# Performance work log

Measured on AMD Instinct MI355X. Metric: run time of the kernel, lower is better.

The kernel has to match this reference:

```python
import jax
import jax.numpy as jnp
from jax import lax
import numpy as np

B, C, Hsp, Wsp = 16, 256, 64, 64
E, HID = 4, 128          # num_experts, expert_hidden
RH = 128                 # router_hidden
TOP_K = 1
EPS = 1e-9


def setup_inputs() -> dict:
    key = jax.random.key(0)
    ks = jax.random.split(key, 8)
    s = lambda *shape: 1.0 / np.sqrt(shape[-1])
    x = jax.random.normal(ks[0], (B, C, Hsp, Wsp), dtype=jnp.float32)
    # router: Linear(C->RH), Linear(RH->E)
    Wr1 = jax.random.normal(ks[1], (RH, C), dtype=jnp.float32) * s(RH, C)
    br1 = jnp.zeros((RH,), dtype=jnp.float32)
    Wr2 = jax.random.normal(ks[2], (E, RH), dtype=jnp.float32) * s(E, RH)
    br2 = jnp.zeros((E,), dtype=jnp.float32)
    # experts (stacked over E): 1x1 C->HID, 3x3 HID->HID, 1x1 HID->C, all bias-free
    W1 = jax.random.normal(ks[3], (E, HID, C), dtype=jnp.float32) * s(E, HID, C)
    W2 = jax.random.normal(ks[4], (E, HID, HID, 3, 3), dtype=jnp.float32) * (1.0 / np.sqrt(HID * 9))
    W3 = jax.random.normal(ks[5], (E, C, HID), dtype=jnp.float32) * s(E, C, HID)
    return {"x": x, "Wr1": Wr1, "br1": br1, "Wr2": Wr2, "br2": br2,
            "W1": W1, "W2": W2, "W3": W3}


def reference(x, Wr1, br1, Wr2, br2, W1, W2, W3):
    b = x.shape[0]
    # --- router on globally pooled features ---
    pooled = x.mean(axis=(2, 3))                      # [B, C]
    h = jax.nn.relu(pooled @ Wr1.T + br1)             # [B, RH]
    logits = h @ Wr2.T + br2                          # [B, E]
    probs = jax.nn.softmax(logits, axis=1)
    # top-k masking + renormalize (top_k < num_experts)
    vals, idx = lax.top_k(probs, TOP_K)               # [B, k]
    mask = jnp.zeros_like(probs).at[jnp.arange(b)[:, None], idx].set(vals)
    probs = mask / (mask.sum(axis=1, keepdims=True) + EPS)
    # --- run all experts (as in original) ---
    # 1x1 conv C->HID, per expert:  [B, E, HID, H, W]
    y1 = jax.nn.relu(jnp.einsum('bcij,ehc->behij', x, W1))
    # 3x3 grouped conv (one group per expert), HID->HID
    y1m = y1.reshape(b, E * HID, Hsp, Wsp)
    y2 = lax.conv_general_dilated(
        y1m, W2.reshape(E * HID, HID, 3, 3),
        window_strides=(1, 1), padding='SAME',
        feature_group_count=E,
        dimension_numbers=('NCHW', 'OIHW', 'NCHW'))
    y2 = jax.nn.relu(y2).reshape(b, E, HID, Hsp, Wsp)
    # 1x1 conv HID->C fused with routed weighted sum over experts + residual
    out = jnp.einsum('begij,ecg,be->bcij', y2, W3, probs) + x
    return out
```

## Files before the change

### kernel.cpp

```cpp
#include <hip/hip_runtime.h>

typedef unsigned short ushort_t;
typedef unsigned int uint32;
typedef __attribute__((ext_vector_type(8))) short s16x8;
typedef __attribute__((ext_vector_type(4))) float f32x4;

#define BB   16
#define CC   256
#define NPX  4096
#define EE   4
#define HID  128
#define RHH  128
#define PW   66
#define PPX  (66*66)

__device__ __forceinline__ ushort_t f2bf(float f) {
  uint32 x = __float_as_uint(f);
  x += 0x7fffu + ((x >> 16) & 1u);
  return (ushort_t)(x >> 16);
}
__device__ __forceinline__ void g2l16(const void* g, void* l) {
  __builtin_amdgcn_global_load_lds((const __attribute__((address_space(1))) uint32*)g,
                                   (__attribute__((address_space(3))) uint32*)l, 16, 0, 0);
}

__global__ __launch_bounds__(256)
void k_xprep(const float* __restrict__ x, ushort_t* __restrict__ xT,
             float* __restrict__ part,
             const float* __restrict__ W1f, const float* __restrict__ W3f,
             const float* __restrict__ W2f, ushort_t* __restrict__ W1b,
             ushort_t* __restrict__ W3b, ushort_t* __restrict__ W2r,
             ushort_t* __restrict__ y1Tp) {
  int bid = blockIdx.x, t = threadIdx.x;
  if (bid < 4096) {
    int pxblk = bid & 63, c0 = ((bid >> 6) & 3) * 64, b = bid >> 8;
    int px0 = pxblk * 64;
    __shared__ float T[64][65];
    const float* xg = x + (size_t)b * CC * NPX;
    int cr = t >> 4, p4 = (t & 15) * 4;
#pragma unroll
    for (int i = 0; i < 4; ++i) {
      float4 v = *(const float4*)(xg + (size_t)(c0 + cr + i * 16) * NPX + px0 + p4);
      T[cr + i * 16][p4 + 0] = v.x; T[cr + i * 16][p4 + 1] = v.y;
      T[cr + i * 16][p4 + 2] = v.z; T[cr + i * 16][p4 + 3] = v.w;
    }
    __syncthreads();
    {
      int c = t >> 2, q = t & 3;
      float s = 0.f;
#pragma unroll
      for (int k = 0; k < 16; ++k) s += T[c][q * 16 + k];
      s += __shfl_down(s, 1, 64);
      s += __shfl_down(s, 2, 64);
      if (q == 0) part[((size_t)b * CC + c0 + c) * 64 + pxblk] = s;
    }
    int px = t >> 2, cg = (t & 3) * 16;
    uint32 o[8];
#pragma unroll
    for (int u = 0; u < 8; ++u) {
      uint32 lo = f2bf(T[cg + 2 * u][px]);
      uint32 hi = f2bf(T[cg + 2 * u + 1][px]);
      o[u] = lo | (hi << 16);
    }
    ushort_t* dst = xT + ((size_t)b * NPX + px0 + px) * CC + c0 + cg;
    *(uint4*)dst = make_uint4(o[0], o[1], o[2], o[3]);
    *(uint4*)(dst + 8) = make_uint4(o[4], o[5], o[6], o[7]);
  } else if (bid < 4352) {
    int i4 = ((bid - 4096) * 256 + t) * 4;
    const float* src; ushort_t* dst; int off;
    if (i4 < EE * HID * CC) { src = W1f; dst = W1b; off = i4; }
    else { src = W3f; dst = W3b; off = i4 - EE * HID * CC; }
    float4 v = *(const float4*)(src + off);
    ushort4 o;
    o.x = f2bf(v.x); o.y = f2bf(v.y); o.z = f2bf(v.z); o.w = f2bf(v.w);
    *(ushort4*)(dst + off) = o;
  } else if (bid < 6656) {
    int i = (bid - 4352) * 256 + t;
    int h = i & 127;
    int g = (i >> 7) & 127;
    int et = i >> 14;
    int tap = et % 9;
    int e = et / 9;
    W2r[i] = f2bf(W2f[((((size_t)e * 128 + g) * 128 + h) * 3 + tap / 3) * 3 + tap % 3]);
  } else {
    int p = (bid - 6656) * 8 + (t >> 5);
    int b = p / 260, i = p % 260;
    int row, col;
    if (i < 66)       { row = 0;       col = i; }
    else if (i < 132) { row = 65;      col = i - 66; }
    else if (i < 196) { row = i - 131; col = 0; }
    else              { row = i - 195; col = 65; }
    uint2* dst = (uint2*)(y1Tp + (((size_t)b * PPX + row * PW + col) * HID) + (t & 31) * 4);
    *dst = make_uint2(0u, 0u);
  }
}

__global__ __launch_bounds__(128)
void k_router(const float* __restrict__ part, const float* __restrict__ Wr1,
              const float* __restrict__ br1, const float* __restrict__ Wr2,
              const float* __restrict__ br2, int* __restrict__ eidx,
              float* __restrict__ gatew) {
  int b = blockIdx.x, t = threadIdx.x;
  __shared__ float spool[CC];
  __shared__ float hb[RHH];
  __shared__ float lg[EE];
  for (int cc = t; cc < CC; cc += 128) {
    const float* pp = part + ((size_t)b * CC + cc) * 64;
    float s = 0.f;
#pragma unroll
    for (int k = 0; k < 64; ++k) s += pp[k];
    spool[cc] = s;
  }
  __syncthreads();
  float s0 = 0.f;
  const float* wr = Wr1 + t * CC;
  for (int c = 0; c < CC; ++c) s0 += spool[c] * wr[c];
  float a = br1[t] + s0 * (1.0f / NPX);
  hb[t] = a > 0.f ? a : 0.f;
  __syncthreads();
  if (t < EE) {
    float s = br2[t];
    const float* w2 = Wr2 + t * RHH;
    for (int r = 0; r < RHH; ++r) s += hb[r] * w2[r];
    lg[t] = s;
  }
  __syncthreads();
  if (t == 0) {
    float m = lg[0]; int mi = 0;
    for (int e = 1; e < EE; ++e) if (lg[e] > m) { m = lg[e]; mi = e; }
    float den = 0.f;
    for (int e = 0; e < EE; ++e) den += expf(lg[e] - m);
    float v = 1.0f / den;
    eidx[b] = mi;
    gatew[b] = v / (v + 1e-9f);
  }
}

#define STAGE64(dstA, srcA_expr, dstB, srcB_expr)                         \
  {                                                                       \
    _Pragma("unroll")                                                     \
    for (int s_ = 0; s_ < 4; ++s_) {                                      \
      int ch_ = wave * 4 + s_;                                            \
      int r = ch_ * 8 + (lane >> 3);                                      \
      int kc = ((lane & 7) ^ (lane >> 3)) * 8;                            \
      g2l16(srcA_expr, &dstA[ch_ * 512]);                                 \
      g2l16(srcB_expr, &dstB[ch_ * 512]);                                 \
    }                                                                     \
  }

#define STAGE64B(dstB, srcB_expr)                                         \
  {                                                                       \
    _Pragma("unroll")                                                     \
    for (int s_ = 0; s_ < 4; ++s_) {                                      \
      int ch_ = wave * 4 + s_;                                            \
      int r = ch_ * 8 + (lane >> 3);                                      \
      int kc = ((lane & 7) ^ (lane >> 3)) * 8;                            \
      g2l16(srcB_expr, &dstB[ch_ * 512]);                                 \
    }                                                                     \
  }

#define MFMA64(At_, Bt_, ACC_)                                            \
  _Pragma("unroll")                                                       \
  for (int kh = 0; kh < 2; ++kh) {                                        \
    s16x8 af[4], bfr[4];                                                  \
    int cidx = ((kh * 4 + (lane >> 4)) ^ (lane & 7)) * 8;                 \
    _Pragma("unroll")                                                     \
    for (int i = 0; i < 4; ++i)                                           \
      af[i] = *(const s16x8*)&At_[(wm + i * 16 + (lane & 15)) * 64 + cidx]; \
    _Pragma("unroll")                                                     \
    for (int j = 0; j < 4; ++j)                                           \
      bfr[j] = *(const s16x8*)&Bt_[(wn + j * 16 + (lane & 15)) * 64 + cidx]; \
    _Pragma("unroll")                                                     \
    for (int i = 0; i < 4; ++i)                                           \
      _Pragma("unroll")                                                   \
      for (int j = 0; j < 4; ++j)                                         \
        ACC_[i][j] = __builtin_amdgcn_mfma_f32_16x16x32_bf16(af[i], bfr[j], ACC_[i][j], 0, 0, 0); \
  }

__global__ __launch_bounds__(256)
void k_conv1(const ushort_t* __restrict__ xT, const ushort_t* __restrict__ W1b,
             const int* __restrict__ eidx, ushort_t* __restrict__ y1Tp) {
  int mt = blockIdx.x, b = blockIdx.y;
  int e = eidx[b];
  int t = threadIdx.x, wave = t >> 6, lane = t & 63;
  int wm = (wave & 1) * 64, wn = (wave >> 1) * 64;
  __shared__ ushort_t At[128 * 64];
  __shared__ ushort_t Bt[128 * 64];
  f32x4 acc[4][4] = {};
  const ushort_t* ab = xT + ((size_t)b * NPX + mt * 128) * CC;
  const ushort_t* w1 = W1b + (size_t)e * HID * CC;

  for (int ks = 0; ks < 4; ++ks) {
    int k0 = ks * 64;
    __syncthreads();
    STAGE64(At, ab + (size_t)r * CC + k0 + kc,
            Bt, w1 + (size_t)r * CC + k0 + kc);
    __syncthreads();
    MFMA64(At, Bt, acc);
  }
  ushort_t* yb = y1Tp + (size_t)b * PPX * HID;
#pragma unroll
  for (int i = 0; i < 4; ++i) {
#pragma unroll
    for (int r = 0; r < 4; ++r) {
      int m = wm + i * 16 + (lane >> 4) * 4 + r;
      int prow = mt * 2 + (m >> 6) + 1;
      int pcol = (m & 63) + 1;
      ushort_t* row = yb + ((size_t)prow * PW + pcol) * HID + wn + (lane & 15);
#pragma unroll
      for (int j = 0; j < 4; ++j) {
        float v = acc[i][j][r];
        row[j * 16] = f2bf(v > 0.f ? v : 0.f);
      }
    }
  }
}

__global__ __launch_bounds__(256, 2)
void k_conv23(const ushort_t* __restrict__ y1Tp, const ushort_t* __restrict__ W2r,
              const ushort_t* __restrict__ W3b, const float* __restrict__ x,
              const int* __restrict__ eidx, const float* __restrict__ gatew,
              float* __restrict__ out) {
  int mt = blockIdx.x, b = blockIdx.y;
  int e = eidx[b];
  float gw = gatew[b];
  int t = threadIdx.x, wave = t >> 6, lane = t & 63;
  int wm = (wave & 1) * 64, wn = (wave >> 1) * 64;
  __shared__ ushort_t bufA[128 * 64];
  __shared__ ushort_t bufB[128 * 64];
  __shared__ ushort_t y2s[2][128 * 64];
  const ushort_t* yb = y1Tp + (size_t)b * PPX * HID;
  const ushort_t* w2e = W2r + (size_t)e * 9 * HID * HID;

  f32x4 acc[4][4] = {};
  for (int tap = 0; tap < 9; ++tap) {
    int dy = tap / 3 - 1, dx = tap % 3 - 1;
    const ushort_t* w2t = w2e + tap * HID * HID;
#pragma unroll
    for (int ks = 0; ks < 2; ++ks) {
      int k0 = ks * 64;
      __syncthreads();
      STAGE64(bufA, yb + ((size_t)(mt * 2 + (r >> 6) + 1 + dy) * PW + (r & 63) + 1 + dx) * HID + k0 + kc,
              bufB, w2t + (size_t)r * HID + k0 + kc);
      __syncthreads();
      MFMA64(bufA, bufB, acc);
    }
  }
#pragma unroll
  for (int i = 0; i < 4; ++i)
#pragma unroll
    for (int j = 0; j < 4; ++j)
#pragma unroll
      for (int r = 0; r < 4; ++r) {
        int m = wm + i * 16 + (lane >> 4) * 4 + r;
        int n = wn + j * 16 + (lane & 15);
        float v = acc[i][j][r];
        ushort_t bv = f2bf(v > 0.f ? v : 0.f);
        int nn = n & 63;
        ushort_t* buf = (n < 64) ? y2s[0] : y2s[1];
        buf[m * 64 + ((nn >> 3) ^ (m & 7)) * 8 + (nn & 7)] = bv;
      }
  __syncthreads();
  f32x4 acc3[2][4][4] = {};
  const ushort_t* w3 = W3b + (size_t)e * CC * HID;
#pragma unroll
  for (int h = 0; h < 2; ++h) {
#pragma unroll
    for (int ks = 0; ks < 2; ++ks) {
      ushort_t* bt = (ks == 0) ? bufA : bufB;
      STAGE64B(bt, w3 + (size_t)(h * 128 + r) * HID + ks * 64 + kc);
      __syncthreads();
      MFMA64(y2s[ks], bt, acc3[h]);
    }
  }
  float* Tf = (float*)y2s;
  for (int h = 0; h < 2; ++h) {
    for (int jj = 0; jj < 4; ++jj) {
      __syncthreads();
      if ((wn >> 6) == (jj >> 1)) {
        int j0 = (jj & 1) * 2;
#pragma unroll
        for (int jd = 0; jd < 2; ++jd) {
          int cl = jd * 16 + (lane & 15);
#pragma unroll
          for (int i = 0; i < 4; ++i) {
            int pb = wm + i * 16 + (lane >> 4) * 4;
            *(f32x4*)&Tf[cl * 132 + pb] = acc3[h][i][j0 + jd];
          }
        }
      }
      __syncthreads();
#pragma unroll
      for (int it = 0; it < 4; ++it) {
        int idx = it * 256 + t;
        int crow = idx >> 5;
        int p4 = (idx & 31) * 4;
        int c = h * 128 + jj * 32 + crow;
        int px = mt * 128 + p4;
        size_t base = ((size_t)b * CC + c) * NPX + px;
        f32x4 vv = *(const f32x4*)&Tf[crow * 132 + p4];
        f32x4 xa = *(const f32x4*)(x + base);
        vv = gw * vv + xa;
        __builtin_nontemporal_store(vv, (f32x4*)(out + base));
      }
    }
  }
}

extern "C" void kernel_launch(void* const* d_in, const int* in_sizes, int n_in,
                              void* d_out, int out_size, void* d_ws, size_t ws_size,
                              hipStream_t stream) {
  const float* x   = (const float*)d_in[0];
  const float* Wr1 = (const float*)d_in[1];
  const float* br1 = (const float*)d_in[2];
  const float* Wr2 = (const float*)d_in[3];
  const float* br2 = (const float*)d_in[4];
  const float* W1  = (const float*)d_in[5];
  const float* W2  = (const float*)d_in[6];
  const float* W3  = (const float*)d_in[7];
  float* out = (float*)d_out;

  char* ws = (char*)d_ws;
  int*      eidx  = (int*)ws;
  float*    gatew = (float*)(ws + 64);
  float*    part  = (float*)(ws + 256);
  ushort_t* W1b   = (ushort_t*)(ws + 1048832);
  ushort_t* W3b   = (ushort_t*)(ws + 1310976);
  ushort_t* W2r   = (ushort_t*)(ws + 1573120);
  ushort_t* y1Tp  = (ushort_t*)(ws + 2752768);
  ushort_t* xT    = (ushort_t*)d_out;

  k_xprep <<<7176, 256, 0, stream>>>(x, xT, part, W1, W3, W2, W1b, W3b, W2r, y1Tp);
  k_router<<<16, 128, 0, stream>>>(part, Wr1, br1, Wr2, br2, eidx, gatew);
  k_conv1 <<<dim3(32, 16), 256, 0, stream>>>(xT, W1b, eidx, y1Tp);
  k_conv23<<<dim3(32, 16), 256, 0, stream>>>(y1Tp, W2r, W3b, x, eidx, gatew, out);
}
```

Measured before the change: 190.8 us.

## Fuse x transpose and bf16 cast into conv1 staging, stage conv1 output via LDS

Removes the separate transposed bf16 copy of x: the prep kernel now only computes per-channel pooled sums, and conv1 reads fp32 x directly, converting and transposing into swizzled LDS tiles. The conv1 epilogue now writes its results to LDS first and then emits coalesced 16-byte stores into the padded y1 buffer. This avoids one full write and read of a 32 MB intermediate. In exchange, conv1 does strided fp32 loads with conversion inside its main loop.

```diff
diff --git a/kernel.cpp b/kernel.cpp
--- a/kernel.cpp
+++ b/kernel.cpp
@@ -25,46 +25,27 @@
 }
 
 __global__ __launch_bounds__(256)
-void k_xprep(const float* __restrict__ x, ushort_t* __restrict__ xT,
-             float* __restrict__ part,
-             const float* __restrict__ W1f, const float* __restrict__ W3f,
-             const float* __restrict__ W2f, ushort_t* __restrict__ W1b,
-             ushort_t* __restrict__ W3b, ushort_t* __restrict__ W2r,
-             ushort_t* __restrict__ y1Tp) {
+void k_prep(const float* __restrict__ x, float* __restrict__ pooled,
+            const float* __restrict__ W1f, const float* __restrict__ W3f,
+            const float* __restrict__ W2f, ushort_t* __restrict__ W1b,
+            ushort_t* __restrict__ W3b, ushort_t* __restrict__ W2r,
+            ushort_t* __restrict__ y1Tp) {
   int bid = blockIdx.x, t = threadIdx.x;
   if (bid < 4096) {
-    int pxblk = bid & 63, c0 = ((bid >> 6) & 3) * 64, b = bid >> 8;
-    int px0 = pxblk * 64;
-    __shared__ float T[64][65];
-    const float* xg = x + (size_t)b * CC * NPX;
-    int cr = t >> 4, p4 = (t & 15) * 4;
-#pragma unroll
-    for (int i = 0; i < 4; ++i) {
-      float4 v = *(const float4*)(xg + (size_t)(c0 + cr + i * 16) * NPX + px0 + p4);
-      T[cr + i * 16][p4 + 0] = v.x; T[cr + i * 16][p4 + 1] = v.y;
-      T[cr + i * 16][p4 + 2] = v.z; T[cr + i * 16][p4 + 3] = v.w;
-    }
+    int c = bid & 255, b = bid >> 8;
+    const float* xg = x + ((size_t)b * CC + c) * NPX;
+    float s = 0.f;
+#pragma unroll
+    for (int k = 0; k < 4; ++k) {
+      float4 v = *(const float4*)(xg + (size_t)(k * 256 + t) * 4);
+      s += v.x + v.y + v.z + v.w;
+    }
+#pragma unroll
+    for (int o = 32; o >= 1; o >>= 1) s += __shfl_down(s, o, 64);
+    __shared__ float wsum[4];
+    if ((t & 63) == 0) wsum[t >> 6] = s;
     __syncthreads();
-    {
-      int c = t >> 2, q = t & 3;
-      float s = 0.f;
-#pragma unroll
-      for (int k = 0; k < 16; ++k) s += T[c][q * 16 + k];
-      s += __shfl_down(s, 1, 64);
-      s += __shfl_down(s, 2, 64);
-      if (q == 0) part[((size_t)b * CC + c0 + c) * 64 + pxblk] = s;
-    }
-    int px = t >> 2, cg = (t & 3) * 16;
-    uint32 o[8];
-#pragma unroll
-    for (int u = 0; u < 8; ++u) {
-      uint32 lo = f2bf(T[cg + 2 * u][px]);
-      uint32 hi = f2bf(T[cg + 2 * u + 1][px]);
-      o[u] = lo | (hi << 16);
-    }
-    ushort_t* dst = xT + ((size_t)b * NPX + px0 + px) * CC + c0 + cg;
-    *(uint4*)dst = make_uint4(o[0], o[1], o[2], o[3]);
-    *(uint4*)(dst + 8) = make_uint4(o[4], o[5], o[6], o[7]);
+    if (t == 0) pooled[(size_t)b * CC + c] = wsum[0] + wsum[1] + wsum[2] + wsum[3];
   } else if (bid < 4352) {
     int i4 = ((bid - 4096) * 256 + t) * 4;
     const float* src; ushort_t* dst; int off;
@@ -96,7 +77,7 @@
 }
 
 __global__ __launch_bounds__(128)
-void k_router(const float* __restrict__ part, const float* __restrict__ Wr1,
+void k_router(const float* __restrict__ pooled, const float* __restrict__ Wr1,
               const float* __restrict__ br1, const float* __restrict__ Wr2,
               const float* __restrict__ br2, int* __restrict__ eidx,
               float* __restrict__ gatew) {
@@ -104,13 +85,7 @@
   __shared__ float spool[CC];
   __shared__ float hb[RHH];
   __shared__ float lg[EE];
-  for (int cc = t; cc < CC; cc += 128) {
-    const float* pp = part + ((size_t)b * CC + cc) * 64;
-    float s = 0.f;
-#pragma unroll
-    for (int k = 0; k < 64; ++k) s += pp[k];
-    spool[cc] = s;
-  }
+  for (int cc = t; cc < CC; cc += 128) spool[cc] = pooled[(size_t)b * CC + cc];
   __syncthreads();
   float s0 = 0.f;
   const float* wr = Wr1 + t * CC;
@@ -178,41 +153,69 @@
   }
 
 __global__ __launch_bounds__(256)
-void k_conv1(const ushort_t* __restrict__ xT, const ushort_t* __restrict__ W1b,
+void k_conv1(const float* __restrict__ x, const ushort_t* __restrict__ W1b,
              const int* __restrict__ eidx, ushort_t* __restrict__ y1Tp) {
   int mt = blockIdx.x, b = blockIdx.y;
   int e = eidx[b];
   int t = threadIdx.x, wave = t >> 6, lane = t & 63;
   int wm = (wave & 1) * 64, wn = (wave >> 1) * 64;
-  __shared__ ushort_t At[128 * 64];
-  __shared__ ushort_t Bt[128 * 64];
+  __shared__ ushort_t smem[128 * 128];
+  ushort_t* At = smem;
+  ushort_t* Bt = smem + 128 * 64;
   f32x4 acc[4][4] = {};
-  const ushort_t* ab = xT + ((size_t)b * NPX + mt * 128) * CC;
+  const float* xg = x + (size_t)b * CC * NPX + mt * 128;
   const ushort_t* w1 = W1b + (size_t)e * HID * CC;
+
+  int cp = t >> 3;
+  int kk = cp * 2;
+  int pxb = (t & 7) * 4;
 
   for (int ks = 0; ks < 4; ++ks) {
     int k0 = ks * 64;
     __syncthreads();
-    STAGE64(At, ab + (size_t)r * CC + k0 + kc,
-            Bt, w1 + (size_t)r * CC + k0 + kc);
+    STAGE64B(Bt, w1 + (size_t)r * CC + k0 + kc);
+    {
+      const float* r0 = xg + (size_t)(k0 + kk) * NPX;
+      const float* r1 = r0 + NPX;
+#pragma unroll
+      for (int i = 0; i < 4; ++i) {
+        int p = pxb + i * 32;
+        float4 va = *(const float4*)(r0 + p);
+        float4 vb = *(const float4*)(r1 + p);
+#pragma unroll
+        for (int q = 0; q < 4; ++q) {
+          int m = p + q;
+          uint32 v = (uint32)f2bf(((const float*)&va)[q]) |
+                     ((uint32)f2bf(((const float*)&vb)[q]) << 16);
+          int us = m * 64 + (((kk >> 3) ^ (m & 7)) << 3) + (kk & 7);
+          *(uint32*)&At[us] = v;
+        }
+      }
+    }
     __syncthreads();
     MFMA64(At, Bt, acc);
   }
+  __syncthreads();
+#pragma unroll
+  for (int i = 0; i < 4; ++i)
+#pragma unroll
+    for (int j = 0; j < 4; ++j)
+#pragma unroll
+      for (int r = 0; r < 4; ++r) {
+        int m = wm + i * 16 + (lane >> 4) * 4 + r;
+        int n = wn + j * 16 + (lane & 15);
+        float v = acc[i][j][r];
+        smem[m * 128 + (((n >> 3) ^ (m & 7)) << 3) + (n & 7)] = f2bf(v > 0.f ? v : 0.f);
+      }
+  __syncthreads();
   ushort_t* yb = y1Tp + (size_t)b * PPX * HID;
 #pragma unroll
-  for (int i = 0; i < 4; ++i) {
-#pragma unroll
-    for (int r = 0; r < 4; ++r) {
-      int m = wm + i * 16 + (lane >> 4) * 4 + r;
-      int prow = mt * 2 + (m >> 6) + 1;
-      int pcol = (m & 63) + 1;
-      ushort_t* row = yb + ((size_t)prow * PW + pcol) * HID + wn + (lane & 15);
-#pragma unroll
-      for (int j = 0; j < 4; ++j) {
-        float v = acc[i][j][r];
-        row[j * 16] = f2bf(v > 0.f ? v : 0.f);
-      }
-    }
+  for (int it = 0; it < 8; ++it) {
+    int idx = it * 256 + t;
+    int row = idx >> 4, ch = idx & 15;
+    int prow = mt * 2 + (row >> 6) + 1, pcol = (row & 63) + 1;
+    uint4 v = *(const uint4*)&smem[row * 128 + ((ch ^ (row & 7)) << 3)];
+    *(uint4*)(yb + ((size_t)prow * PW + pcol) * HID + ch * 8) = v;
   }
 }
 
@@ -321,17 +324,16 @@
   float* out = (float*)d_out;
 
   char* ws = (char*)d_ws;
-  int*      eidx  = (int*)ws;
-  float*    gatew = (float*)(ws + 64);
-  float*    part  = (float*)(ws + 256);
-  ushort_t* W1b   = (ushort_t*)(ws + 1048832);
-  ushort_t* W3b   = (ushort_t*)(ws + 1310976);
-  ushort_t* W2r   = (ushort_t*)(ws + 1573120);
-  ushort_t* y1Tp  = (ushort_t*)(ws + 2752768);
-  ushort_t* xT    = (ushort_t*)d_out;
-
-  k_xprep <<<7176, 256, 0, stream>>>(x, xT, part, W1, W3, W2, W1b, W3b, W2r, y1Tp);
-  k_router<<<16, 128, 0, stream>>>(part, Wr1, br1, Wr2, br2, eidx, gatew);
-  k_conv1 <<<dim3(32, 16), 256, 0, stream>>>(xT, W1b, eidx, y1Tp);
+  int*      eidx   = (int*)ws;
+  float*    gatew  = (float*)(ws + 64);
+  float*    pooled = (float*)(ws + 256);
+  ushort_t* W1b    = (ushort_t*)(ws + 16640);
+  ushort_t* W3b    = (ushort_t*)(ws + 278784);
+  ushort_t* W2r    = (ushort_t*)(ws + 540928);
+  ushort_t* y1Tp   = (ushort_t*)(ws + 1720576);
+
+  k_prep  <<<7176, 256, 0, stream>>>(x, pooled, W1, W3, W2, W1b, W3b, W2r, y1Tp);
+  k_router<<<16, 128, 0, stream>>>(pooled, Wr1, br1, Wr2, br2, eidx, gatew);
+  k_conv1 <<<dim3(32, 16), 256, 0, stream>>>(x, W1b, eidx, y1Tp);
   k_conv23<<<dim3(32, 16), 256, 0, stream>>>(y1Tp, W2r, W3b, x, eidx, gatew, out);
 }
```

Result: faster. 186.7 us (-2.2%).
